# Performance work log

Measured on AMD Instinct MI355X. Metric: run time of the kernel, lower is better.

## Reference

```python
import jax, jax.numpy as jnp
import numpy as np

V, D, H, L, RATIO, T_MAX = 1024, 512, 8, 11, 3, 1024
DH = D // H
HID = D * RATIO
NB, DB = 2048, 128  # bigram buckets / dim
EPS = 1e-6


def _rope_tables(T):
    pos = jnp.arange(T, dtype=jnp.float32)
    freqs = 1.0 / (10000.0 ** (jnp.arange(0, DH, 2, dtype=jnp.float32) / DH))
    emb = jnp.outer(pos, freqs)  # [T, DH/2]
    return jnp.cos(emb), jnp.sin(emb)


def _rmsnorm(x, w):
    return x * jax.lax.rsqrt(jnp.mean(x * x, axis=-1, keepdims=True) + EPS) * w


def setup_inputs() -> dict:
    key = jax.random.key(0)
    ks = jax.random.split(key, 10)
    B, T = 8, 1024
    s = 0.02
    return {
        "x": jax.random.randint(ks[0], (B, T), 0, V),
        "embed": jax.random.normal(ks[1], (V, D), jnp.float32) * s,
        "Wqkv": jax.random.normal(ks[2], (L, 3 * D, D), jnp.float32) * s,
        "Wproj": jax.random.normal(ks[3], (L, D, D), jnp.float32) * s,
        "n1_w": jnp.ones((L, D), jnp.float32),
        "n2_w": jnp.ones((L, D), jnp.float32),
        "Wfc1": jax.random.normal(ks[4], (L, HID, D), jnp.float32) * s,
        "Wfc2": jax.random.normal(ks[5], (L, D, HID), jnp.float32) * s,
        "norm_f_w": jnp.ones((D,), jnp.float32),
        "bg_embed": jax.random.normal(ks[6], (NB, DB), jnp.float32) * s,
        "bg_proj": jax.random.normal(ks[7], (V, DB), jnp.float32) * s,
    }


def _attn(x, Wqkv, Wproj, cos, sin, causal):
    B, T, C = x.shape
    qkv = x @ Wqkv.T  # [B,T,3D]
    q, k, v = jnp.split(qkv, 3, axis=-1)
    def heads(t):
        return t.reshape(B, T, H, DH).transpose(0, 2, 1, 3)  # [B,H,T,DH]
    q, k, v = heads(q), heads(k), heads(v)
    c = cos[None, None]  # [1,1,T,DH/2]
    s = sin[None, None]
    def rope(t):
        t1, t2 = t[..., : DH // 2], t[..., DH // 2 :]
        return jnp.concatenate([t1 * c - t2 * s, t1 * s + t2 * c], axis=-1)
    q, k = rope(q), rope(k)
    w = jnp.einsum("bhqd,bhkd->bhqk", q, k) * (DH ** -0.5)
    w = jnp.where(causal, w, -jnp.inf)
    w = jax.nn.softmax(w.astype(jnp.float32), axis=-1).astype(x.dtype)
    out = jnp.einsum("bhqk,bhkd->bhqd", w, v)
    self_w = jnp.diagonal(w, axis1=-2, axis2=-1)[..., None]  # [B,H,T,1]
    out = out - self_w * v  # XSA: subtract self-value contribution
    out = out.transpose(0, 2, 1, 3).reshape(B, T, C)
    return out @ Wproj.T


def reference(x, embed, Wqkv, Wproj, n1_w, n2_w, Wfc1, Wfc2, norm_f_w, bg_embed, bg_proj):
    B, T = x.shape
    cos, sin = _rope_tables(T_MAX)
    cos, sin = cos[:T], sin[:T]
    causal = jnp.tril(jnp.ones((T, T), dtype=bool))
    # bigram logits from previous token
    prev = jnp.concatenate([jnp.zeros((B, 1), x.dtype), x[:, :-1]], axis=1)
    bigram_logits = bg_embed[prev % NB] @ bg_proj.T  # [B,T,V]
    h = embed[x]
    for i in range(L):
        h = h + _attn(_rmsnorm(h, n1_w[i]), Wqkv[i], Wproj[i], cos, sin, causal)
        z = _rmsnorm(h, n2_w[i])
        h = h + jnp.square(jax.nn.relu(z @ Wfc1[i].T)) @ Wfc2[i].T
    h = _rmsnorm(h, norm_f_w)
    return h @ embed.T + bigram_logits
```

## Files before the change

### kernel.cpp

```cpp
#include <hip/hip_runtime.h>

#define NROW   8192
#define DMODEL 512
#define TSEQ   1024
#define LAYERS 11
#define HIDDEN 1536

typedef __bf16 bf16_t;
typedef bf16_t bf16x8 __attribute__((ext_vector_type(8)));
typedef bf16_t bf16x4 __attribute__((ext_vector_type(4)));
typedef float  f32x4  __attribute__((ext_vector_type(4)));
typedef unsigned int u32;
typedef u32 u32x4 __attribute__((ext_vector_type(4)));

#define GLD16(gp, lp) __builtin_amdgcn_global_load_lds( \
    (const __attribute__((address_space(1))) void*)(gp), \
    (__attribute__((address_space(3))) void*)(lp), 16, 0, 0)

#if __has_builtin(__builtin_amdgcn_exp2f)
#define EXP2(x) __builtin_amdgcn_exp2f(x)
#else
#define EXP2(x) exp2f(x)
#endif

__global__ void rope_table_k(float* __restrict__ cosT, float* __restrict__ sinT) {
    int i = blockIdx.x * blockDim.x + threadIdx.x;
    int t = i >> 5, j = i & 31;
    float freq = powf(10000.f, -(float)j * (1.f / 32.f));
    float ang = (float)t * freq;
    cosT[i] = cosf(ang);
    sinT[i] = sinf(ang);
}

__global__ void embed_gather_k(const int* __restrict__ x,
                               const float* __restrict__ embed,
                               float* __restrict__ h) {
    int n = blockIdx.x;
    int d = threadIdx.x;
    const float4* e = (const float4*)(embed + (size_t)x[n] * DMODEL);
    float4* hp = (float4*)(h + (size_t)n * DMODEL);
    hp[d] = e[d];
}

__global__ void bg_gather_k(const int* __restrict__ x,
                            const float* __restrict__ bge,
                            bf16_t* __restrict__ Afu) {
    int n = blockIdx.x;
    int t = n & (TSEQ - 1);
    int prev = (t == 0) ? 0 : x[n - 1];
    Afu[(size_t)n * 640 + 512 + threadIdx.x] = (bf16_t)bge[(size_t)prev * 128 + threadIdx.x];
}

__global__ void cvt_bf16_k(const float* __restrict__ in, bf16_t* __restrict__ out, int n8) {
    int i = blockIdx.x * blockDim.x + threadIdx.x;
    if (i >= n8) return;
    float4 a = ((const float4*)in)[2 * i];
    float4 b = ((const float4*)in)[2 * i + 1];
    bf16x8 o;
    o[0] = (bf16_t)a.x; o[1] = (bf16_t)a.y; o[2] = (bf16_t)a.z; o[3] = (bf16_t)a.w;
    o[4] = (bf16_t)b.x; o[5] = (bf16_t)b.y; o[6] = (bf16_t)b.z; o[7] = (bf16_t)b.w;
    ((bf16x8*)out)[i] = o;
}

__global__ void cvt_pad_k(const float* __restrict__ in, bf16_t* __restrict__ out,
                          int n8, int lshift, int mask, int colOff) {
    int i = blockIdx.x * blockDim.x + threadIdx.x;
    if (i >= n8) return;
    int i8 = i * 8;
    int row = i8 >> lshift;
    int col = i8 & mask;
    float4 a = ((const float4*)in)[2 * i];
    float4 b = ((const float4*)in)[2 * i + 1];
    bf16x8 o;
    o[0] = (bf16_t)a.x; o[1] = (bf16_t)a.y; o[2] = (bf16_t)a.z; o[3] = (bf16_t)a.w;
    o[4] = (bf16_t)b.x; o[5] = (bf16_t)b.y; o[6] = (bf16_t)b.z; o[7] = (bf16_t)b.w;
    *(bf16x8*)&out[(size_t)row * 640 + colOff + col] = o;
}

__global__ __launch_bounds__(256) void rmsnorm_k(const float* __restrict__ in,
                                                 const float* __restrict__ w,
                                                 bf16_t* __restrict__ out,
                                                 int ostride) {
    int wv = threadIdx.x >> 6, lane = threadIdx.x & 63;
    int row = (blockIdx.x << 2) + wv;
    const float* rp = in + (size_t)row * DMODEL + lane * 8;
    float4 v0 = *(const float4*)(rp);
    float4 v1 = *(const float4*)(rp + 4);
    float ss = v0.x*v0.x + v0.y*v0.y + v0.z*v0.z + v0.w*v0.w
             + v1.x*v1.x + v1.y*v1.y + v1.z*v1.z + v1.w*v1.w;
#pragma unroll
    for (int off = 32; off; off >>= 1) ss += __shfl_xor(ss, off, 64);
    float sc = rsqrtf(ss * (1.f / DMODEL) + 1e-6f);
    const float* wp = w + lane * 8;
    float4 w0 = *(const float4*)(wp);
    float4 w1 = *(const float4*)(wp + 4);
    bf16x8 o;
    o[0] = (bf16_t)(v0.x * sc * w0.x); o[1] = (bf16_t)(v0.y * sc * w0.y);
    o[2] = (bf16_t)(v0.z * sc * w0.z); o[3] = (bf16_t)(v0.w * sc * w0.w);
    o[4] = (bf16_t)(v1.x * sc * w1.x); o[5] = (bf16_t)(v1.y * sc * w1.y);
    o[6] = (bf16_t)(v1.z * sc * w1.z); o[7] = (bf16_t)(v1.w * sc * w1.w);
    *(bf16x8*)(out + (size_t)row * ostride + lane * 8) = o;
}

template<int BM, int EPI>
__global__ __launch_bounds__(256, 2)
void gemm_mfma(const bf16_t* __restrict__ A,
               const bf16_t* __restrict__ B,
               float* __restrict__ Cf,
               bf16_t* __restrict__ Cb,
               const float* __restrict__ cosT,
               const float* __restrict__ sinT,
               int M, int N, int K, int nbx) {
    constexpr int NT  = 256;
    constexpr int WM  = 2;
    constexpr int MI  = BM / WM / 16;
    constexpr int ACH = (BM * 4) / NT;
    constexpr int BCH = 2;
    __shared__ __align__(16) bf16_t As[3][BM * 32];
    __shared__ __align__(16) bf16_t Bs[3][128 * 32];
    const int tid = threadIdx.x;
    const int w = tid >> 6, lane = tid & 63;

    const int nwg = (int)gridDim.x;
    const int bid = blockIdx.x;
    const int swz = (bid & 7) * (nwg >> 3) + (bid >> 3);
    const int bx = swz % nbx, by = swz / nbx;

    const int m0 = by * BM, n0 = bx * 128;
    const int wr = (w >> 1) * (BM / WM), wc = (w & 1) * 64;
    const int fr = lane & 15, fq = lane >> 4;

    f32x4 acc[MI][4] = {};

    float cold[EPI == 1 ? MI : 1][4][4];
    if constexpr (EPI == 1) {
#pragma unroll
        for (int i = 0; i < MI; ++i)
#pragma unroll
            for (int j = 0; j < 4; ++j)
#pragma unroll
                for (int q = 0; q < 4; ++q)
                    cold[i][j][q] = Cf[(size_t)(m0 + wr + i * 16 + fq * 4 + q) * N
                                       + n0 + wc + j * 16 + fr];
    }

    auto stage = [&](int k0, int buf) {
#pragma unroll
        for (int c = 0; c < ACH; ++c) {
            int idx = c * NT + tid;
            int row = idx >> 2, cs = idx & 3;
            GLD16(A + (size_t)(m0 + row) * K + k0 + cs * 8,
                  &As[buf][(size_t)(c * NT + w * 64) * 8]);
        }
#pragma unroll
        for (int c = 0; c < BCH; ++c) {
            int idx = c * NT + tid;
            int row = idx >> 2, cs = idx & 3;
            GLD16(B + (size_t)(n0 + row) * K + k0 + cs * 8,
                  &Bs[buf][(size_t)(c * NT + w * 64) * 8]);
        }
    };

    const int NK = K >> 5;
    stage(0, 0);
    stage(32, 1);
    for (int k = 0; k < NK; ++k) {
        const int cur = k % 3;
        if (k + 2 < NK) {
            stage((k + 2) << 5, (k + 2) % 3);
            if constexpr (BM == 128) asm volatile("s_waitcnt vmcnt(8)" ::: "memory");
            else                     asm volatile("s_waitcnt vmcnt(6)" ::: "memory");
        } else if (k + 1 < NK) {
            if constexpr (BM == 128) asm volatile("s_waitcnt vmcnt(4)" ::: "memory");
            else                     asm volatile("s_waitcnt vmcnt(3)" ::: "memory");
        } else {
            asm volatile("s_waitcnt vmcnt(0)" ::: "memory");
        }
        __builtin_amdgcn_s_barrier();
        __builtin_amdgcn_sched_barrier(0);

        bf16x8 a[MI], b[4];
        const bf16_t* ap = &As[cur][(size_t)(wr + fr) * 32 + fq * 8];
        const bf16_t* bp = &Bs[cur][(size_t)(wc + fr) * 32 + fq * 8];
#pragma unroll
        for (int i = 0; i < MI; ++i) a[i] = *(const bf16x8*)(ap + i * 16 * 32);
#pragma unroll
        for (int j = 0; j < 4; ++j)  b[j] = *(const bf16x8*)(bp + j * 16 * 32);
        __builtin_amdgcn_s_setprio(1);
#pragma unroll
        for (int i = 0; i < MI; ++i)
#pragma unroll
            for (int j = 0; j < 4; ++j)
                acc[i][j] = __builtin_amdgcn_mfma_f32_16x16x32_bf16(a[i], b[j], acc[i][j], 0, 0, 0);
        __builtin_amdgcn_s_setprio(0);

        asm volatile("s_waitcnt lgkmcnt(0)" ::: "memory");
        __builtin_amdgcn_s_barrier();
        __builtin_amdgcn_sched_barrier(0);
    }

    if (EPI == 4) {
        const bool qk = (n0 + wc) < 1024;
#pragma unroll
        for (int i = 0; i < MI; ++i) {
#pragma unroll
            for (int q = 0; q < 4; ++q) {
                int row = m0 + wr + i * 16 + fq * 4 + q;
                size_t rb = (size_t)row * N + n0 + wc;
                if (qk) {
                    int t = row & (TSEQ - 1);
#pragma unroll
                    for (int j = 0; j < 2; ++j) {
                        int d = j * 16 + fr;
                        float c = cosT[t * 32 + d];
                        float s = sinT[t * 32 + d];
                        float v1 = acc[i][j][q], v2 = acc[i][j + 2][q];
                        Cb[rb + j * 16 + fr]       = (bf16_t)(v1 * c - v2 * s);
                        Cb[rb + (j + 2) * 16 + fr] = (bf16_t)(v1 * s + v2 * c);
                    }
                } else {
#pragma unroll
                    for (int j = 0; j < 4; ++j)
                        Cb[rb + j * 16 + fr] = (bf16_t)acc[i][j][q];
                }
            }
        }
        return;
    }
#pragma unroll
    for (int i = 0; i < MI; ++i) {
        int row = m0 + wr + i * 16 + fq * 4;
#pragma unroll
        for (int j = 0; j < 4; ++j) {
            int col = n0 + wc + j * 16 + fr;
#pragma unroll
            for (int q = 0; q < 4; ++q) {
                float v = acc[i][j][q];
                size_t off = (size_t)(row + q) * N + col;
                if (EPI == 0)      Cf[off] = v;
                else if (EPI == 1) Cf[off] = cold[i][j][q] + v;
                else if (EPI == 2) { v = fmaxf(v, 0.f); Cb[off] = (bf16_t)(v * v); }
            }
        }
    }
}

__global__ __launch_bounds__(256) void attn_mfma_k(const bf16_t* __restrict__ qkvb,
                                                   bf16_t* __restrict__ outb) {
    __shared__ __align__(16) bf16_t Ks[2][64 * 64];
    __shared__ __align__(16) bf16_t VsT[2][2 * 64 * 32];

    const int tid = threadIdx.x;
    const int w  = tid >> 6;
    const int ln = tid & 63;
    const int lr = ln & 15;
    const int lg = ln >> 4;

    const int bid = blockIdx.x;
    const int qb = 15 - (bid >> 6);
    const int bh = bid & 63;
    const int b = bh >> 3, h = bh & 7;
    const int tq0b = qb << 6;
    const int tq0  = tq0b + w * 16;
    const int qrow = tq0 + lr;

    const bf16_t* Qg = qkvb + (size_t)b * TSEQ * 1536 + h * 64;
    const bf16_t* Kg = Qg + 512;
    const bf16_t* Vg = Qg + 1024;

    const int mk = tid >> 4;
    const int md = tid & 15;
    const int src0 = lr + 32 * (lg & 1);
    const int fsel = lg >> 1;
    const int gofs = 8 * (lg ^ ((lr >> 2) & 3));

    auto KSTAGE = [&](int t0, int buf) {
#pragma unroll
        for (int ii = 0; ii < 2; ++ii) {
            const int i = w * 2 + ii;
            int key = i * 8 + (ln >> 3);
            int dc  = (ln & 7) ^ (ln >> 3);
            GLD16(Kg + (size_t)(t0 + key) * 1536 + dc * 8, &Ks[buf][i * 512]);
        }
    };
    auto VLOAD = [&](int t0, bf16x4* rv) {
#pragma unroll
        for (int i = 0; i < 4; ++i)
            rv[i] = *(const bf16x4*)(Vg + (size_t)(t0 + mk * 4 + i) * 1536 + md * 4);
    };
    auto VWRITE = [&](const bf16x4* rv, int buf) {
        const int s = mk >> 3;
#pragma unroll
        for (int j = 0; j < 4; ++j) {
            int row = md * 4 + j;
            bf16x4 wv;
            wv[0] = rv[0][j]; wv[1] = rv[1][j]; wv[2] = rv[2][j]; wv[3] = rv[3][j];
            int g = (mk & 7) ^ ((md & 3) << 1);
            *(bf16x4*)&VsT[buf][s * 2048 + row * 32 + g * 4] = wv;
        }
    };

    bf16x8 qreg[2];
    {
        const float QS = 0.1803368801f;
        const bf16_t* qp = Qg + (size_t)qrow * 1536 + lg * 8;
        qreg[0] = *(const bf16x8*)qp;
        qreg[1] = *(const bf16x8*)(qp + 32);
#pragma unroll
        for (int j = 0; j < 8; ++j) {
            qreg[0][j] = (bf16_t)((float)qreg[0][j] * QS);
            qreg[1][j] = (bf16_t)((float)qreg[1][j] * QS);
        }
    }

    f32x4 accO[4] = {};
    float mrun = -1e30f, pl = 0.f, esf = 0.f;

    {
        bf16x4 rv[4];
        KSTAGE(0, 0);
        VLOAD(0, rv);
        asm volatile("s_waitcnt vmcnt(0)" ::: "memory");
        VWRITE(rv, 0);
        asm volatile("s_waitcnt lgkmcnt(0)" ::: "memory");
        __builtin_amdgcn_s_barrier();
        __builtin_amdgcn_sched_barrier(0);
    }

    for (int t0 = 0; t0 <= tq0b; t0 += 64) {
        const int cur = (t0 >> 6) & 1;
        const bool more = t0 < tq0b;
        const bool masked = t0 == tq0b;
        bf16x4 rv[4];
        if (more) {
            KSTAGE(t0 + 64, cur ^ 1);
            VLOAD(t0 + 64, rv);
        }

        f32x4 sq[4] = {};
        __builtin_amdgcn_s_setprio(1);
#pragma unroll
        for (int kr = 0; kr < 4; ++kr) {
            int key = kr * 16 + lr;
#pragma unroll
            for (int s = 0; s < 2; ++s) {
                int chunk = key * 8 + ((s * 4 + lg) ^ (key & 7));
                bf16x8 kf = *(const bf16x8*)&Ks[cur][chunk * 8];
                sq[kr] = __builtin_amdgcn_mfma_f32_16x16x32_bf16(kf, qreg[s], sq[kr], 0, 0, 0);
            }
        }
        __builtin_amdgcn_s_setprio(0);

        float e16[4][4];
        float tm = -1e30f;
        if (masked) {
#pragma unroll
            for (int f = 0; f < 4; ++f)
#pragma unroll
                for (int r = 0; r < 4; ++r) {
                    int key = t0 + f * 16 + lg * 4 + r;
                    float sv = (key <= qrow) ? sq[f][r] : -1e30f;
                    e16[f][r] = sv;
                    tm = fmaxf(tm, sv);
                }
        } else {
#pragma unroll
            for (int f = 0; f < 4; ++f)
#pragma unroll
                for (int r = 0; r < 4; ++r) {
                    e16[f][r] = sq[f][r];
                    tm = fmaxf(tm, sq[f][r]);
                }
        }
        tm = fmaxf(tm, __shfl_xor(tm, 16, 64));
        tm = fmaxf(tm, __shfl_xor(tm, 32, 64));

        const bool resc = __any(tm > mrun + 8.f);
        float mnew = resc ? fmaxf(mrun, tm) : mrun;
        float psum = 0.f;
#pragma unroll
        for (int f = 0; f < 4; ++f)
#pragma unroll
            for (int r = 0; r < 4; ++r) {
                float e = EXP2(e16[f][r] - mnew);
                e16[f][r] = e;
                psum += e;
            }
        float pd = 0.f;
        if (masked) {
#pragma unroll
            for (int f = 0; f < 4; ++f)
#pragma unroll
                for (int r = 0; r < 4; ++r) {
                    int key = t0 + f * 16 + lg * 4 + r;
                    pd = (key == qrow) ? e16[f][r] : pd;
                }
        }
        if (resc) {
            float corr = EXP2(mrun - mnew);
            mrun = mnew;
            pl  = pl  * corr + psum;
            esf = esf * corr + pd;
#pragma unroll
            for (int dblk = 0; dblk < 4; ++dblk)
#pragma unroll
                for (int r = 0; r < 4; ++r) accO[dblk][r] *= corr;
        } else {
            pl  += psum;
            esf += pd;
        }

        u32 plo[4], phi[4];
#pragma unroll
        for (int f = 0; f < 4; ++f) {
            bf16x4 t;
            t[0] = (bf16_t)e16[f][0]; t[1] = (bf16_t)e16[f][1];
            t[2] = (bf16_t)e16[f][2]; t[3] = (bf16_t)e16[f][3];
            uint2 pr = __builtin_bit_cast(uint2, t);
            plo[f] = pr.x; phi[f] = pr.y;
        }

#pragma unroll
        for (int s = 0; s < 2; ++s) {
            u32 a0 = (u32)__shfl((int)plo[s * 2],     src0,      64);
            u32 a1 = (u32)__shfl((int)phi[s * 2],     src0,      64);
            u32 a2 = (u32)__shfl((int)plo[s * 2],     src0 + 16, 64);
            u32 a3 = (u32)__shfl((int)phi[s * 2],     src0 + 16, 64);
            u32 c0 = (u32)__shfl((int)plo[s * 2 + 1], src0,      64);
            u32 c1 = (u32)__shfl((int)phi[s * 2 + 1], src0,      64);
            u32 c2 = (u32)__shfl((int)plo[s * 2 + 1], src0 + 16, 64);
            u32 c3 = (u32)__shfl((int)phi[s * 2 + 1], src0 + 16, 64);
            u32x4 bw;
            bw[0] = fsel ? c0 : a0;
            bw[1] = fsel ? c1 : a1;
            bw[2] = fsel ? c2 : a2;
            bw[3] = fsel ? c3 : a3;
            bf16x8 bfrag = __builtin_bit_cast(bf16x8, bw);
            __builtin_amdgcn_s_setprio(1);
#pragma unroll
            for (int dblk = 0; dblk < 4; ++dblk) {
                bf16x8 av = *(const bf16x8*)&VsT[cur][s * 2048 + (dblk * 16 + lr) * 32 + gofs];
                accO[dblk] = __builtin_amdgcn_mfma_f32_16x16x32_bf16(av, bfrag, accO[dblk], 0, 0, 0);
            }
            __builtin_amdgcn_s_setprio(0);
        }

        if (more) {
            asm volatile("s_waitcnt vmcnt(0)" ::: "memory");
            VWRITE(rv, cur ^ 1);
            asm volatile("s_waitcnt lgkmcnt(0)" ::: "memory");
            __builtin_amdgcn_s_barrier();
            __builtin_amdgcn_sched_barrier(0);
        }
    }

    pl  += __shfl_xor(pl, 16, 64);  pl  += __shfl_xor(pl, 32, 64);
    esf += __shfl_xor(esf, 16, 64); esf += __shfl_xor(esf, 32, 64);
    float rin = 1.0f / pl;
    const bf16_t* vqp = Vg + (size_t)qrow * 1536;
    bf16_t* op = outb + (size_t)(b * TSEQ + qrow) * DMODEL + h * 64;
#pragma unroll
    for (int dblk = 0; dblk < 4; ++dblk) {
        bf16x4 vq = *(const bf16x4*)(vqp + dblk * 16 + lg * 4);
        bf16x4 o4;
#pragma unroll
        for (int r = 0; r < 4; ++r)
            o4[r] = (bf16_t)((accO[dblk][r] - esf * (float)vq[r]) * rin);
        *(bf16x4*)(op + dblk * 16 + lg * 4) = o4;
    }
}

static inline void cvt(const float* in, bf16_t* out, size_t n, hipStream_t s) {
    int n8 = (int)(n / 8);
    cvt_bf16_k<<<(n8 + 255) / 256, 256, 0, s>>>(in, out, n8);
}

extern "C" void kernel_launch(void* const* d_in, const int* in_sizes, int n_in,
                              void* d_out, int out_size, void* d_ws, size_t ws_size,
                              hipStream_t stream) {
    const int*   x     = (const int*)d_in[0];
    const float* embed = (const float*)d_in[1];
    const float* Wqkv  = (const float*)d_in[2];
    const float* Wproj = (const float*)d_in[3];
    const float* n1w   = (const float*)d_in[4];
    const float* n2w   = (const float*)d_in[5];
    const float* Wfc1  = (const float*)d_in[6];
    const float* Wfc2  = (const float*)d_in[7];
    const float* normf = (const float*)d_in[8];
    const float* bge   = (const float*)d_in[9];
    const float* bgp   = (const float*)d_in[10];
    float* out = (float*)d_out;

    float* ws   = (float*)d_ws;
    float* cosT = ws;
    float* sinT = cosT + 32768;
    float* h    = sinT + 32768;
    bf16_t* qkvb = (bf16_t*)(h + (size_t)NROW * DMODEL);
    bf16_t* ub   = qkvb;
    bf16_t* Afu  = qkvb;
    bf16_t* xn   = qkvb + (size_t)NROW * 1536;
    bf16_t* atb  = xn  + (size_t)NROW * DMODEL;
    bf16_t* wqb  = atb + (size_t)NROW * DMODEL;
    bf16_t* wpb  = wqb + (size_t)LAYERS * 3 * DMODEL * DMODEL;
    bf16_t* w1b  = wpb + (size_t)LAYERS * DMODEL * DMODEL;
    bf16_t* w2b  = w1b + (size_t)LAYERS * HIDDEN * DMODEL;
    bf16_t* bfu  = w2b + (size_t)LAYERS * DMODEL * HIDDEN;

    rope_table_k<<<128, 256, 0, stream>>>(cosT, sinT);
    embed_gather_k<<<NROW, 128, 0, stream>>>(x, embed, h);

    cvt(Wqkv,  wqb,  (size_t)LAYERS * 3 * DMODEL * DMODEL, stream);
    cvt(Wproj, wpb,  (size_t)LAYERS * DMODEL * DMODEL, stream);
    cvt(Wfc1,  w1b,  (size_t)LAYERS * HIDDEN * DMODEL, stream);
    cvt(Wfc2,  w2b,  (size_t)LAYERS * DMODEL * HIDDEN, stream);
    cvt_pad_k<<<(65536 + 255) / 256, 256, 0, stream>>>(embed, bfu, 65536, 9, 511, 0);
    cvt_pad_k<<<(16384 + 255) / 256, 256, 0, stream>>>(bgp,   bfu, 16384, 7, 127, 512);

    for (int i = 0; i < LAYERS; ++i) {
        rmsnorm_k<<<NROW / 4, 256, 0, stream>>>(h, n1w + i * DMODEL, xn, DMODEL);
        gemm_mfma<128, 4><<<768, 256, 0, stream>>>(
            xn, wqb + (size_t)i * 3 * DMODEL * DMODEL, nullptr, qkvb,
            cosT, sinT, NROW, 3 * DMODEL, DMODEL, 12);
        attn_mfma_k<<<1024, 256, 0, stream>>>(qkvb, atb);
        gemm_mfma<64, 1><<<512, 256, 0, stream>>>(
            atb, wpb + (size_t)i * DMODEL * DMODEL, h, nullptr,
            nullptr, nullptr, NROW, DMODEL, DMODEL, 4);
        rmsnorm_k<<<NROW / 4, 256, 0, stream>>>(h, n2w + i * DMODEL, xn, DMODEL);
        gemm_mfma<128, 2><<<768, 256, 0, stream>>>(
            xn, w1b + (size_t)i * HIDDEN * DMODEL, nullptr, ub,
            nullptr, nullptr, NROW, HIDDEN, DMODEL, 12);
        gemm_mfma<64, 1><<<512, 256, 0, stream>>>(
            ub, w2b + (size_t)i * DMODEL * HIDDEN, h, nullptr,
            nullptr, nullptr, NROW, DMODEL, HIDDEN, 4);
    }

    rmsnorm_k<<<NROW / 4, 256, 0, stream>>>(h, normf, Afu, 640);
    bg_gather_k<<<NROW, 128, 0, stream>>>(x, bge, Afu);
    gemm_mfma<64, 0><<<1024, 256, 0, stream>>>(
        Afu, bfu, out, nullptr, nullptr, nullptr, NROW, 1024, 640, 8);
}
```

Measured before the change: 1.512 ms.

## Fold RMSNorm weights into GEMM weights and apply row scale in epilogue

Folds the n1/n2 RMSNorm gains into the bf16 Wqkv and Wfc1 weights at conversion time. The residual GEMMs now also write a bf16 copy of h, so each layer's norm shrinks to a small kernel that computes one rsqrt scale per row. That scale is applied in the QKV and FC1 epilogues, removing the full normalized-activation write/read per norm. The change also switches the final logits GEMM to a 128-row tile. The cost is an extra bf16 store in the residual epilogues, plus a slight numerics change because the norm scale is computed from the bf16 copy of h.

```diff
diff --git a/kernel.cpp b/kernel.cpp
--- a/kernel.cpp
+++ b/kernel.cpp
@@ -34,12 +34,15 @@
 
 __global__ void embed_gather_k(const int* __restrict__ x,
                                const float* __restrict__ embed,
-                               float* __restrict__ h) {
+                               float* __restrict__ h,
+                               bf16_t* __restrict__ hb) {
     int n = blockIdx.x;
     int d = threadIdx.x;
-    const float4* e = (const float4*)(embed + (size_t)x[n] * DMODEL);
-    float4* hp = (float4*)(h + (size_t)n * DMODEL);
-    hp[d] = e[d];
+    float4 v = ((const float4*)(embed + (size_t)x[n] * DMODEL))[d];
+    ((float4*)(h + (size_t)n * DMODEL))[d] = v;
+    bf16x4 o;
+    o[0] = (bf16_t)v.x; o[1] = (bf16_t)v.y; o[2] = (bf16_t)v.z; o[3] = (bf16_t)v.w;
+    *(bf16x4*)(hb + (size_t)n * DMODEL + d * 4) = o;
 }
 
 __global__ void bg_gather_k(const int* __restrict__ x,
@@ -59,6 +62,27 @@
     bf16x8 o;
     o[0] = (bf16_t)a.x; o[1] = (bf16_t)a.y; o[2] = (bf16_t)a.z; o[3] = (bf16_t)a.w;
     o[4] = (bf16_t)b.x; o[5] = (bf16_t)b.y; o[6] = (bf16_t)b.z; o[7] = (bf16_t)b.w;
+    ((bf16x8*)out)[i] = o;
+}
+
+__global__ void cvt_fold_k(const float* __restrict__ in,
+                           const float* __restrict__ nw,
+                           bf16_t* __restrict__ out, int n8, int layerSz) {
+    int i = blockIdx.x * blockDim.x + threadIdx.x;
+    if (i >= n8) return;
+    int i8 = i * 8;
+    int k = i8 & 511;
+    int l = i8 / layerSz;
+    const float* wv = nw + l * DMODEL + k;
+    float4 a = ((const float4*)in)[2 * i];
+    float4 b = ((const float4*)in)[2 * i + 1];
+    float4 wa = *(const float4*)wv;
+    float4 wb = *(const float4*)(wv + 4);
+    bf16x8 o;
+    o[0] = (bf16_t)(a.x * wa.x); o[1] = (bf16_t)(a.y * wa.y);
+    o[2] = (bf16_t)(a.z * wa.z); o[3] = (bf16_t)(a.w * wa.w);
+    o[4] = (bf16_t)(b.x * wb.x); o[5] = (bf16_t)(b.y * wb.y);
+    o[6] = (bf16_t)(b.z * wb.z); o[7] = (bf16_t)(b.w * wb.w);
     ((bf16x8*)out)[i] = o;
 }
 
@@ -77,6 +101,19 @@
     *(bf16x8*)&out[(size_t)row * 640 + colOff + col] = o;
 }
 
+__global__ __launch_bounds__(256) void scale_k(const bf16_t* __restrict__ hb,
+                                               float* __restrict__ s) {
+    int wv = threadIdx.x >> 6, lane = threadIdx.x & 63;
+    int row = (blockIdx.x << 2) + wv;
+    bf16x8 v = *(const bf16x8*)(hb + (size_t)row * DMODEL + lane * 8);
+    float ss = 0.f;
+#pragma unroll
+    for (int j = 0; j < 8; ++j) { float f = (float)v[j]; ss += f * f; }
+#pragma unroll
+    for (int off = 32; off; off >>= 1) ss += __shfl_xor(ss, off, 64);
+    if (lane == 0) s[row] = rsqrtf(ss * (1.f / DMODEL) + 1e-6f);
+}
+
 __global__ __launch_bounds__(256) void rmsnorm_k(const float* __restrict__ in,
                                                  const float* __restrict__ w,
                                                  bf16_t* __restrict__ out,
@@ -110,12 +147,14 @@
                bf16_t* __restrict__ Cb,
                const float* __restrict__ cosT,
                const float* __restrict__ sinT,
+               const float* __restrict__ Sc,
                int M, int N, int K, int nbx) {
     constexpr int NT  = 256;
     constexpr int WM  = 2;
     constexpr int MI  = BM / WM / 16;
     constexpr int ACH = (BM * 4) / NT;
     constexpr int BCH = 2;
+    constexpr bool SCALED = (EPI == 2 || EPI == 4);
     __shared__ __align__(16) bf16_t As[3][BM * 32];
     __shared__ __align__(16) bf16_t Bs[3][128 * 32];
     const int tid = threadIdx.x;
@@ -132,6 +171,14 @@
 
     f32x4 acc[MI][4] = {};
 
+    float sld[SCALED ? MI : 1][4];
+    if constexpr (SCALED) {
+#pragma unroll
+        for (int i = 0; i < MI; ++i)
+#pragma unroll
+            for (int q = 0; q < 4; ++q)
+                sld[i][q] = Sc[m0 + wr + i * 16 + fq * 4 + q];
+    }
     float cold[EPI == 1 ? MI : 1][4][4];
     if constexpr (EPI == 1) {
 #pragma unroll
@@ -207,6 +254,7 @@
             for (int q = 0; q < 4; ++q) {
                 int row = m0 + wr + i * 16 + fq * 4 + q;
                 size_t rb = (size_t)row * N + n0 + wc;
+                float sm = sld[i][q];
                 if (qk) {
                     int t = row & (TSEQ - 1);
 #pragma unroll
@@ -214,14 +262,14 @@
                         int d = j * 16 + fr;
                         float c = cosT[t * 32 + d];
                         float s = sinT[t * 32 + d];
-                        float v1 = acc[i][j][q], v2 = acc[i][j + 2][q];
+                        float v1 = acc[i][j][q] * sm, v2 = acc[i][j + 2][q] * sm;
                         Cb[rb + j * 16 + fr]       = (bf16_t)(v1 * c - v2 * s);
                         Cb[rb + (j + 2) * 16 + fr] = (bf16_t)(v1 * s + v2 * c);
                     }
                 } else {
 #pragma unroll
                     for (int j = 0; j < 4; ++j)
-                        Cb[rb + j * 16 + fr] = (bf16_t)acc[i][j][q];
+                        Cb[rb + j * 16 + fr] = (bf16_t)(acc[i][j][q] * sm);
                 }
             }
         }
@@ -238,8 +286,14 @@
                 float v = acc[i][j][q];
                 size_t off = (size_t)(row + q) * N + col;
                 if (EPI == 0)      Cf[off] = v;
-                else if (EPI == 1) Cf[off] = cold[i][j][q] + v;
-                else if (EPI == 2) { v = fmaxf(v, 0.f); Cb[off] = (bf16_t)(v * v); }
+                else if (EPI == 1) {
+                    float nv = cold[i][j][q] + v;
+                    Cf[off] = nv;
+                    Cb[off] = (bf16_t)nv;
+                } else if (EPI == 2) {
+                    v = fmaxf(v * sld[i][q], 0.f);
+                    Cb[off] = (bf16_t)(v * v);
+                }
             }
         }
     }
@@ -498,44 +552,49 @@
     bf16_t* qkvb = (bf16_t*)(h + (size_t)NROW * DMODEL);
     bf16_t* ub   = qkvb;
     bf16_t* Afu  = qkvb;
-    bf16_t* xn   = qkvb + (size_t)NROW * 1536;
-    bf16_t* atb  = xn  + (size_t)NROW * DMODEL;
+    bf16_t* hb   = qkvb + (size_t)NROW * 1536;
+    bf16_t* atb  = hb  + (size_t)NROW * DMODEL;
     bf16_t* wqb  = atb + (size_t)NROW * DMODEL;
     bf16_t* wpb  = wqb + (size_t)LAYERS * 3 * DMODEL * DMODEL;
     bf16_t* w1b  = wpb + (size_t)LAYERS * DMODEL * DMODEL;
     bf16_t* w2b  = w1b + (size_t)LAYERS * HIDDEN * DMODEL;
     bf16_t* bfu  = w2b + (size_t)LAYERS * DMODEL * HIDDEN;
+    float*  sbuf = (float*)(bfu + (size_t)1024 * 640);
 
     rope_table_k<<<128, 256, 0, stream>>>(cosT, sinT);
-    embed_gather_k<<<NROW, 128, 0, stream>>>(x, embed, h);
-
-    cvt(Wqkv,  wqb,  (size_t)LAYERS * 3 * DMODEL * DMODEL, stream);
-    cvt(Wproj, wpb,  (size_t)LAYERS * DMODEL * DMODEL, stream);
-    cvt(Wfc1,  w1b,  (size_t)LAYERS * HIDDEN * DMODEL, stream);
-    cvt(Wfc2,  w2b,  (size_t)LAYERS * DMODEL * HIDDEN, stream);
+    embed_gather_k<<<NROW, 128, 0, stream>>>(x, embed, h, hb);
+
+    {
+        int n8q = (int)((size_t)LAYERS * 3 * DMODEL * DMODEL / 8);
+        cvt_fold_k<<<(n8q + 255) / 256, 256, 0, stream>>>(Wqkv, n1w, wqb, n8q, 3 * DMODEL * DMODEL);
+        int n81 = (int)((size_t)LAYERS * HIDDEN * DMODEL / 8);
+        cvt_fold_k<<<(n81 + 255) / 256, 256, 0, stream>>>(Wfc1, n2w, w1b, n81, HIDDEN * DMODEL);
+    }
+    cvt(Wproj, wpb, (size_t)LAYERS * DMODEL * DMODEL, stream);
+    cvt(Wfc2,  w2b, (size_t)LAYERS * DMODEL * HIDDEN, stream);
     cvt_pad_k<<<(65536 + 255) / 256, 256, 0, stream>>>(embed, bfu, 65536, 9, 511, 0);
     cvt_pad_k<<<(16384 + 255) / 256, 256, 0, stream>>>(bgp,   bfu, 16384, 7, 127, 512);
 
     for (int i = 0; i < LAYERS; ++i) {
-        rmsnorm_k<<<NROW / 4, 256, 0, stream>>>(h, n1w + i * DMODEL, xn, DMODEL);
+        scale_k<<<NROW / 4, 256, 0, stream>>>(hb, sbuf);
         gemm_mfma<128, 4><<<768, 256, 0, stream>>>(
-            xn, wqb + (size_t)i * 3 * DMODEL * DMODEL, nullptr, qkvb,
-            cosT, sinT, NROW, 3 * DMODEL, DMODEL, 12);
+            hb, wqb + (size_t)i * 3 * DMODEL * DMODEL, nullptr, qkvb,
+            cosT, sinT, sbuf, NROW, 3 * DMODEL, DMODEL, 12);
         attn_mfma_k<<<1024, 256, 0, stream>>>(qkvb, atb);
         gemm_mfma<64, 1><<<512, 256, 0, stream>>>(
-            atb, wpb + (size_t)i * DMODEL * DMODEL, h, nullptr,
-            nullptr, nullptr, NROW, DMODEL, DMODEL, 4);
-        rmsnorm_k<<<NROW / 4, 256, 0, stream>>>(h, n2w + i * DMODEL, xn, DMODEL);
+            atb, wpb + (size_t)i * DMODEL * DMODEL, h, hb,
+            nullptr, nullptr, nullptr, NROW, DMODEL, DMODEL, 4);
+        scale_k<<<NROW / 4, 256, 0, stream>>>(hb, sbuf);
         gemm_mfma<128, 2><<<768, 256, 0, stream>>>(
-            xn, w1b + (size_t)i * HIDDEN * DMODEL, nullptr, ub,
-            nullptr, nullptr, NROW, HIDDEN, DMODEL, 12);
+            hb, w1b + (size_t)i * HIDDEN * DMODEL, nullptr, ub,
+            nullptr, nullptr, sbuf, NROW, HIDDEN, DMODEL, 12);
         gemm_mfma<64, 1><<<512, 256, 0, stream>>>(
-            ub, w2b + (size_t)i * DMODEL * HIDDEN, h, nullptr,
-            nullptr, nullptr, NROW, DMODEL, HIDDEN, 4);
+            ub, w2b + (size_t)i * DMODEL * HIDDEN, h, hb,
+            nullptr, nullptr, nullptr, NROW, DMODEL, HIDDEN, 4);
     }
 
     rmsnorm_k<<<NROW / 4, 256, 0, stream>>>(h, normf, Afu, 640);
     bg_gather_k<<<NROW, 128, 0, stream>>>(x, bge, Afu);
-    gemm_mfma<64, 0><<<1024, 256, 0, stream>>>(
-        Afu, bfu, out, nullptr, nullptr, nullptr, NROW, 1024, 640, 8);
-}
+    gemm_mfma<128, 0><<<512, 256, 0, stream>>>(
+        Afu, bfu, out, nullptr, nullptr, nullptr, nullptr, NROW, 1024, 640, 8);
+}
```

Result: no change. 1.499 ms (-0.9%).
